# Kernel tuning notes

Hardware: AMD Instinct MI355X
Metric: run time of the kernel (lower is better)

The kernel has to match this reference:

```python
import jax, jax.numpy as jnp
import numpy as np

N_USERS = 100000
N_ITEMS = 50000
N = N_USERS + N_ITEMS
D = 64
N_LAYERS = 3
E = 3000000


def setup_inputs() -> dict:
    key = jax.random.key(0)
    k1, k2, k3, k4, k5 = jax.random.split(key, 5)
    rows = jax.random.randint(k1, (E,), 0, N, dtype=jnp.int32)
    cols = jax.random.randint(k2, (E,), 0, N, dtype=jnp.int32)
    vals = jax.random.uniform(k3, (E,), dtype=jnp.float32)
    user_emb = jax.random.normal(k4, (N_USERS, D), dtype=jnp.float32) * 0.1
    item_emb = jax.random.normal(k5, (N_ITEMS, D), dtype=jnp.float32) * 0.1
    return {"rows": rows, "cols": cols, "vals": vals,
            "user_emb": user_emb, "item_emb": item_emb}


def _spmm(rows, cols, vals, x):
    # sparse (COO) @ dense: out[r] += vals[e] * x[cols[e]]
    msgs = vals[:, None] * x[cols]  # [E, D]
    return jax.ops.segment_sum(msgs, rows, num_segments=N)


def reference(rows, cols, vals, user_emb, item_emb):
    all_emb = jnp.concatenate([user_emb, item_emb], axis=0)  # [N, D]
    acc = all_emb  # running sum over layer outputs (incl. layer 0)
    for _ in range(N_LAYERS):
        all_emb = _spmm(rows, cols, vals, all_emb)
        acc = acc + all_emb
    light_out = acc / (N_LAYERS + 1)  # mean over stacked layer embeddings
    users_final = light_out[:N_USERS]
    items_final = light_out[N_USERS:]
    return users_final, items_final
```

## Files before the change

### kernel.cpp

```cpp
#include <hip/hip_runtime.h>
#include <hip/hip_fp16.h>

#define N_USERS 100000
#define N_ITEMS 50000
#define N_TOT   150000
#define DIM     64
#define E_EDGES 3000000
#define NP1     (N_TOT + 1)
#define NB1     586
#define EPB     4096
#define SEDGE_MAX 4100000

__device__ __forceinline__ __half2 h2_from_int(int x) {
    union { int i; __half2 h; } u; u.i = x; return u.h;
}
__device__ __forceinline__ int int_from_h2(__half2 h) {
    union { int i; __half2 h; } u; u.h = h; return u.i;
}


__global__ void init_kernel(const float* __restrict__ user_emb,
                            const float* __restrict__ item_emb,
                            __half2* __restrict__ b0) {
    int i = blockIdx.x * blockDim.x + threadIdx.x;
    const int total4 = N_TOT * DIM / 4;
    if (i < total4) {
        int base = i * 4;
        float4 v = (base < N_USERS * DIM)
                     ? reinterpret_cast<const float4*>(user_emb)[i]
                     : reinterpret_cast<const float4*>(item_emb)[(base - N_USERS * DIM) >> 2];
        b0[i * 2]     = __floats2half2_rn(v.x, v.y);
        b0[i * 2 + 1] = __floats2half2_rn(v.z, v.w);
    }
}

__global__ void zero_int_kernel(int* __restrict__ p, int n) {
    int i = blockIdx.x * blockDim.x + threadIdx.x;
    if (i < n) p[i] = 0;
}


__global__ __launch_bounds__(256) void hist1_kernel(const int* __restrict__ rows,
                                                    int* __restrict__ hist1) {
    __shared__ int h[NB1];
    for (int b = threadIdx.x; b < NB1; b += 256) h[b] = 0;
    __syncthreads();
    int e0 = blockIdx.x * EPB;
    int cnt = min(EPB, E_EDGES - e0);
    for (int i = threadIdx.x; i < cnt; i += 256)
        atomicAdd(&h[rows[e0 + i] >> 8], 1);
    __syncthreads();
    for (int b = threadIdx.x; b < NB1; b += 256)
        if (h[b]) atomicAdd(&hist1[b], h[b]);
}

__global__ __launch_bounds__(256) void scan586_kernel(const int* __restrict__ src,
                                                      int* __restrict__ dst) {
    __shared__ int psum[256];
    int t = threadIdx.x;
    int i0 = t * 3;
    int s0 = (i0     < NB1) ? src[i0]     : 0;
    int s1 = (i0 + 1 < NB1) ? src[i0 + 1] : 0;
    int s2 = (i0 + 2 < NB1) ? src[i0 + 2] : 0;
    int tsum = s0 + s1 + s2;
    psum[t] = tsum;
    __syncthreads();
    for (int off = 1; off < 256; off <<= 1) {
        int x = (t >= off) ? psum[t - off] : 0;
        __syncthreads();
        psum[t] += x;
        __syncthreads();
    }
    int excl = psum[t] - tsum;
    if (i0     < NB1) dst[i0]     = excl;
    if (i0 + 1 < NB1) dst[i0 + 1] = excl + s0;
    if (i0 + 2 < NB1) dst[i0 + 2] = excl + s0 + s1;
    if (t == 255) dst[NB1] = psum[255];
}

__global__ __launch_bounds__(256) void bin_kernel(const int* __restrict__ rows,
                                                  const int* __restrict__ cols,
                                                  const float* __restrict__ vals,
                                                  const int* __restrict__ bstart,
                                                  int* __restrict__ fill1,
                                                  int2* __restrict__ tmp) {
    __shared__ int sw0[EPB];
    __shared__ int sw1[EPB];
    __shared__ unsigned short sbkt[EPB];
    __shared__ int hist[NB1];
    __shared__ int sstart[NB1];
    __shared__ int gbase[NB1];
    __shared__ int cursor[NB1];
    __shared__ int psum[256];

    int e0 = blockIdx.x * EPB;
    int cnt = min(EPB, E_EDGES - e0);

    for (int b = threadIdx.x; b < NB1; b += 256) hist[b] = 0;
    __syncthreads();

    int r[16], c[16]; float v[16];
#pragma unroll
    for (int k = 0; k < 16; ++k) {
        int i = threadIdx.x + k * 256;
        r[k] = -1;
        if (i < cnt) {
            int e = e0 + i;
            r[k] = rows[e];
            c[k] = cols[e];
            v[k] = vals[e];
            atomicAdd(&hist[r[k] >> 8], 1);
        }
    }
    __syncthreads();

    int t = threadIdx.x;
    int i0 = t * 3;
    int s0 = (i0     < NB1) ? hist[i0]     : 0;
    int s1 = (i0 + 1 < NB1) ? hist[i0 + 1] : 0;
    int s2 = (i0 + 2 < NB1) ? hist[i0 + 2] : 0;
    int tsum = s0 + s1 + s2;
    psum[t] = tsum;
    __syncthreads();
    for (int off = 1; off < 256; off <<= 1) {
        int x = (t >= off) ? psum[t - off] : 0;
        __syncthreads();
        psum[t] += x;
        __syncthreads();
    }
    int excl = psum[t] - tsum;
    if (i0     < NB1) sstart[i0]     = excl;
    if (i0 + 1 < NB1) sstart[i0 + 1] = excl + s0;
    if (i0 + 2 < NB1) sstart[i0 + 2] = excl + s0 + s1;
    __syncthreads();

    for (int b = threadIdx.x; b < NB1; b += 256) {
        int h = hist[b];
        gbase[b] = (h > 0) ? (bstart[b] + atomicAdd(&fill1[b], h)) : 0;
        cursor[b] = sstart[b];
    }
    __syncthreads();

#pragma unroll
    for (int k = 0; k < 16; ++k) {
        if (r[k] >= 0) {
            int b = r[k] >> 8;
            int p = atomicAdd(&cursor[b], 1);
            sw0[p] = ((r[k] & 0xFF) << 24) | c[k];
            sw1[p] = int_from_h2(__floats2half2_rn(v[k], v[k]));
            sbkt[p] = (unsigned short)b;
        }
    }
    __syncthreads();

    for (int i = threadIdx.x; i < cnt; i += 256) {
        int b = sbkt[i];
        int dest = gbase[b] + (i - sstart[b]);
        tmp[dest] = make_int2(sw0[i], sw1[i]);
    }
}

__global__ __launch_bounds__(256) void bukhist_kernel(const int2* __restrict__ tmp,
                                                      const int* __restrict__ bstart,
                                                      int* __restrict__ rowdeg,
                                                      int* __restrict__ bktpad) {
    int b = blockIdx.x;
    int beg = bstart[b], end = bstart[b + 1];
    __shared__ int hist[256];
    __shared__ int sp[256];
    int t = threadIdx.x;
    hist[t] = 0;
    __syncthreads();
    for (int i = beg + t; i < end; i += 256)
        atomicAdd(&hist[((unsigned)tmp[i].x) >> 24], 1);
    __syncthreads();
    int d = hist[t];
    int r = b * 256 + t;
    if (r < N_TOT) rowdeg[r] = d;
    sp[t] = (d + 7) & ~7;
    __syncthreads();
    for (int off = 128; off > 0; off >>= 1) {
        if (t < off) sp[t] += sp[t + off];
        __syncthreads();
    }
    if (t == 0) bktpad[b] = sp[0];
}

__global__ __launch_bounds__(256) void rowptr_kernel(const int* __restrict__ rowdeg,
                                                     const int* __restrict__ pbstart,
                                                     int* __restrict__ row_ptr,
                                                     int2* __restrict__ sedge) {
    int b = blockIdx.x, t = threadIdx.x;
    int r = b * 256 + t;
    int d = (r < N_TOT) ? rowdeg[r] : 0;
    int pd = (d + 7) & ~7;
    __shared__ int scn[256];
    scn[t] = pd;
    __syncthreads();
    for (int off = 1; off < 256; off <<= 1) {
        int x = (t >= off) ? scn[t - off] : 0;
        __syncthreads();
        scn[t] += x;
        __syncthreads();
    }
    int excl = scn[t] - pd;
    int rp = pbstart[b] + excl;
    if (r <= N_TOT) row_ptr[r] = rp;
    if (r < N_TOT) {
        int2* spad = sedge + rp + d;
        for (int i = d; i < pd; ++i) *spad++ = make_int2(0, 0);
    }
}

__global__ __launch_bounds__(256) void sort_kernel(const int2* __restrict__ tmp,
                                                   const int* __restrict__ bstart,
                                                   const int* __restrict__ row_ptr,
                                                   int2* __restrict__ sedge) {
    int b = blockIdx.x;
    int beg = bstart[b], end = bstart[b + 1];
    __shared__ int cursor[256];
    int t = threadIdx.x;
    int r = b * 256 + t;
    cursor[t] = (r < N_TOT) ? row_ptr[r] : 0;
    __syncthreads();
    for (int i = beg + t; i < end; i += 256) {
        int2 rec = tmp[i];
        int lr = ((unsigned)rec.x) >> 24;
        int p = atomicAdd(&cursor[lr], 1);
        sedge[p] = make_int2(rec.x & 0xFFFFFF, rec.y);
    }
}


__global__ __launch_bounds__(256) void spmm2_kernel(const int* __restrict__ row_ptr,
                                                    const int2* __restrict__ sedge,
                                                    const __half2* __restrict__ src,
                                                    __half2* __restrict__ dst,
                                                    const __half2* __restrict__ c0,
                                                    const __half2* __restrict__ c1,
                                                    float* __restrict__ acc,
                                                    int last) {
    int wid2 = (blockIdx.x * blockDim.x + threadIdx.x) >> 6;
    int lane = threadIdx.x & 63;
    int sub = lane & 31;
    int row = wid2 * 2 + (lane >> 5);
    if (row >= N_TOT) return;
    int beg = row_ptr[row];
    int ng  = (row_ptr[row + 1] - beg) >> 3;
    const int4* ep = reinterpret_cast<const int4*>(sedge + beg);
    float s0 = 0.0f, s1 = 0.0f;
    const __half2 z2 = __floats2half2_rn(0.0f, 0.0f);
    for (int g = 0; g < ng; ++g) {
        int4 e0 = ep[0]; int4 e1 = ep[1]; int4 e2 = ep[2]; int4 e3 = ep[3];
        ep += 4;
        __half2 a0 = z2, a1 = z2;
        a0 = __hfma2(h2_from_int(e0.y), src[(unsigned)e0.x * 32u + sub], a0);
        a1 = __hfma2(h2_from_int(e0.w), src[(unsigned)e0.z * 32u + sub], a1);
        a0 = __hfma2(h2_from_int(e1.y), src[(unsigned)e1.x * 32u + sub], a0);
        a1 = __hfma2(h2_from_int(e1.w), src[(unsigned)e1.z * 32u + sub], a1);
        a0 = __hfma2(h2_from_int(e2.y), src[(unsigned)e2.x * 32u + sub], a0);
        a1 = __hfma2(h2_from_int(e2.w), src[(unsigned)e2.z * 32u + sub], a1);
        a0 = __hfma2(h2_from_int(e3.y), src[(unsigned)e3.x * 32u + sub], a0);
        a1 = __hfma2(h2_from_int(e3.w), src[(unsigned)e3.z * 32u + sub], a1);
        float2 fa = __half22float2(__hadd2(a0, a1));
        s0 += fa.x; s1 += fa.y;
    }
    unsigned o = (unsigned)row * 32u + sub;
    if (last) {
        float2 f0 = __half22float2(c0[o]);
        float2 f1 = __half22float2(c1[o]);
        float2 f2 = __half22float2(src[o]);
        float2 rr;
        rr.x = (f0.x + f1.x + f2.x + s0) * 0.25f;
        rr.y = (f0.y + f1.y + f2.y + s1) * 0.25f;
        reinterpret_cast<float2*>(acc)[o] = rr;
    } else {
        dst[o] = __floats2half2_rn(s0, s1);
    }
}


__global__ void initf_kernel(const float* __restrict__ user_emb,
                             const float* __restrict__ item_emb,
                             float* __restrict__ cur,
                             float* __restrict__ acc) {
    int i = blockIdx.x * blockDim.x + threadIdx.x;
    const int total = N_TOT * DIM;
    if (i < total) {
        float v = (i < N_USERS * DIM) ? user_emb[i] : item_emb[i - N_USERS * DIM];
        cur[i] = v;
        acc[i] = v;
    }
}

__global__ void zero_f_kernel(float* __restrict__ p, int n) {
    int i = blockIdx.x * blockDim.x + threadIdx.x;
    if (i < n) p[i] = 0.0f;
}

__global__ void spmm_atomic_kernel(const int* __restrict__ rows, const int* __restrict__ cols,
                                   const float* __restrict__ vals,
                                   const float* __restrict__ cur, float* __restrict__ next) {
    int tid = blockIdx.x * blockDim.x + threadIdx.x;
    int e = tid >> 4;
    int q = (tid & 15) << 2;
    if (e < E_EDGES) {
        int r = rows[e];
        int c = cols[e];
        float v = vals[e];
        const float4 x = *reinterpret_cast<const float4*>(cur + (size_t)c * DIM + q);
        float* dstp = next + (size_t)r * DIM + q;
        atomicAdd(dstp + 0, v * x.x);
        atomicAdd(dstp + 1, v * x.y);
        atomicAdd(dstp + 2, v * x.z);
        atomicAdd(dstp + 3, v * x.w);
    }
}

__global__ void accum_kernel(float* __restrict__ acc, const float* __restrict__ next, int n) {
    int i = blockIdx.x * blockDim.x + threadIdx.x;
    if (i < n) acc[i] += next[i];
}

__global__ void scale_kernel(float* __restrict__ acc, int n) {
    int i = blockIdx.x * blockDim.x + threadIdx.x;
    if (i < n) acc[i] *= 0.25f;
}


extern "C" void kernel_launch(void* const* d_in, const int* in_sizes, int n_in,
                              void* d_out, int out_size, void* d_ws, size_t ws_size,
                              hipStream_t stream) {
    const int*   rows     = (const int*)d_in[0];
    const int*   cols     = (const int*)d_in[1];
    const float* vals     = (const float*)d_in[2];
    const float* user_emb = (const float*)d_in[3];
    const float* item_emb = (const float*)d_in[4];
    float* acc = (float*)d_out;

    const int total  = N_TOT * DIM;
    const int total2 = total / 2;
    const int tb = 256;

    __half2* b0 = (__half2*)d_ws;
    __half2* b1 = b0 + (size_t)total2;
    __half2* b2 = b1 + (size_t)total2;
    int2* tmp   = (int2*)d_ws;
    int2* sedge = (int2*)(b2 + (size_t)total2);
    int* row_ptr = (int*)(sedge + (size_t)SEDGE_MAX);
    int* rowdeg  = row_ptr + NP1;
    int* hist1   = rowdeg + N_TOT;
    int* fill1   = hist1 + NB1;
    int* bktpad  = fill1 + NB1;
    int* bstart  = bktpad + NB1;
    int* pbstart = bstart + NB1 + 1;
    size_t need = (size_t)((char*)(pbstart + NB1 + 1) - (char*)d_ws);

    const int grid_bin = (E_EDGES + EPB - 1) / EPB;

    if (ws_size >= need) {
        zero_int_kernel<<<(2 * NB1 + tb - 1) / tb, tb, 0, stream>>>(hist1, 2 * NB1);
        hist1_kernel<<<grid_bin, tb, 0, stream>>>(rows, hist1);
        scan586_kernel<<<1, tb, 0, stream>>>(hist1, bstart);
        bin_kernel<<<grid_bin, tb, 0, stream>>>(rows, cols, vals, bstart, fill1, tmp);
        bukhist_kernel<<<NB1, tb, 0, stream>>>(tmp, bstart, rowdeg, bktpad);
        scan586_kernel<<<1, tb, 0, stream>>>(bktpad, pbstart);
        rowptr_kernel<<<NB1, tb, 0, stream>>>(rowdeg, pbstart, row_ptr, sedge);
        sort_kernel<<<NB1, tb, 0, stream>>>(tmp, bstart, row_ptr, sedge);

        dim3 blkInit((total / 4 + tb - 1) / tb);
        init_kernel<<<blkInit, tb, 0, stream>>>(user_emb, item_emb, b0);

        const int waves = N_TOT / 2;
        dim3 blkRows((waves * 64 + tb - 1) / tb);
        spmm2_kernel<<<blkRows, tb, 0, stream>>>(row_ptr, sedge, b0, b1, b0, b0, acc, 0);
        spmm2_kernel<<<blkRows, tb, 0, stream>>>(row_ptr, sedge, b1, b2, b0, b0, acc, 0);
        spmm2_kernel<<<blkRows, tb, 0, stream>>>(row_ptr, sedge, b2, b2, b0, b1, acc, 1);
    } else {
        float* fcur = (float*)d_ws;
        float* fnxt = fcur + (size_t)total;
        dim3 blkTotal((total + tb - 1) / tb);
        initf_kernel<<<blkTotal, tb, 0, stream>>>(user_emb, item_emb, fcur, acc);
        const long long spmm_threads = (long long)E_EDGES * 16;
        dim3 blkSpmm((unsigned)((spmm_threads + tb - 1) / tb));
        for (int layer = 0; layer < 3; ++layer) {
            zero_f_kernel<<<blkTotal, tb, 0, stream>>>(fnxt, total);
            spmm_atomic_kernel<<<blkSpmm, tb, 0, stream>>>(rows, cols, vals, fcur, fnxt);
            accum_kernel<<<blkTotal, tb, 0, stream>>>(acc, fnxt, total);
            float* t = fcur; fcur = fnxt; fnxt = t;
        }
        scale_kernel<<<blkTotal, tb, 0, stream>>>(acc, total);
    }
}
```

Baseline: 299.4 us.

## Split sorted edges into column and half-value arrays, fuse rowptr with sort

Sorted edge storage changes from interleaved int2 (column plus duplicated half2 value) to separate int column and __half value arrays, cutting per-edge bytes from 8 to 6. The rowptr and sort kernels are merged into one kernel, dropping a launch and a re-read of row_ptr. The SpMM inner loop now handles two 8-edge groups per iteration with all 16 gathers issued before the FMAs, to expose more memory parallelism. The cost is extra value unpacking via low/high half broadcasts and higher register pressure.

```diff
diff --git a/kernel.cpp b/kernel.cpp
--- a/kernel.cpp
+++ b/kernel.cpp
@@ -10,13 +10,6 @@
 #define NB1     586
 #define EPB     4096
 #define SEDGE_MAX 4100000
-
-__device__ __forceinline__ __half2 h2_from_int(int x) {
-    union { int i; __half2 h; } u; u.i = x; return u.h;
-}
-__device__ __forceinline__ int int_from_h2(__half2 h) {
-    union { int i; __half2 h; } u; u.h = h; return u.i;
-}
 
 
 __global__ void init_kernel(const float* __restrict__ user_emb,
@@ -147,7 +140,7 @@
             int b = r[k] >> 8;
             int p = atomicAdd(&cursor[b], 1);
             sw0[p] = ((r[k] & 0xFF) << 24) | c[k];
-            sw1[p] = int_from_h2(__floats2half2_rn(v[k], v[k]));
+            sw1[p] = __float_as_int(v[k]);
             sbkt[p] = (unsigned short)b;
         }
     }
@@ -186,15 +179,19 @@
     if (t == 0) bktpad[b] = sp[0];
 }
 
-__global__ __launch_bounds__(256) void rowptr_kernel(const int* __restrict__ rowdeg,
-                                                     const int* __restrict__ pbstart,
-                                                     int* __restrict__ row_ptr,
-                                                     int2* __restrict__ sedge) {
+__global__ __launch_bounds__(256) void fsort_kernel(const int* __restrict__ rowdeg,
+                                                    const int* __restrict__ pbstart,
+                                                    const int* __restrict__ bstart,
+                                                    const int2* __restrict__ tmp,
+                                                    int* __restrict__ row_ptr,
+                                                    int* __restrict__ scol,
+                                                    __half* __restrict__ sval) {
     int b = blockIdx.x, t = threadIdx.x;
     int r = b * 256 + t;
     int d = (r < N_TOT) ? rowdeg[r] : 0;
     int pd = (d + 7) & ~7;
     __shared__ int scn[256];
+    __shared__ int cursor[256];
     scn[t] = pd;
     __syncthreads();
     for (int off = 1; off < 256; off <<= 1) {
@@ -206,34 +203,28 @@
     int excl = scn[t] - pd;
     int rp = pbstart[b] + excl;
     if (r <= N_TOT) row_ptr[r] = rp;
+    cursor[t] = rp;
     if (r < N_TOT) {
-        int2* spad = sedge + rp + d;
-        for (int i = d; i < pd; ++i) *spad++ = make_int2(0, 0);
-    }
-}
-
-__global__ __launch_bounds__(256) void sort_kernel(const int2* __restrict__ tmp,
-                                                   const int* __restrict__ bstart,
-                                                   const int* __restrict__ row_ptr,
-                                                   int2* __restrict__ sedge) {
-    int b = blockIdx.x;
+        for (int i = d; i < pd; ++i) {
+            scol[rp + i] = 0;
+            sval[rp + i] = __float2half_rn(0.0f);
+        }
+    }
+    __syncthreads();
     int beg = bstart[b], end = bstart[b + 1];
-    __shared__ int cursor[256];
-    int t = threadIdx.x;
-    int r = b * 256 + t;
-    cursor[t] = (r < N_TOT) ? row_ptr[r] : 0;
-    __syncthreads();
     for (int i = beg + t; i < end; i += 256) {
         int2 rec = tmp[i];
         int lr = ((unsigned)rec.x) >> 24;
         int p = atomicAdd(&cursor[lr], 1);
-        sedge[p] = make_int2(rec.x & 0xFFFFFF, rec.y);
+        scol[p] = rec.x & 0xFFFFFF;
+        sval[p] = __float2half_rn(__int_as_float(rec.y));
     }
 }
 
 
 __global__ __launch_bounds__(256) void spmm2_kernel(const int* __restrict__ row_ptr,
-                                                    const int2* __restrict__ sedge,
+                                                    const int* __restrict__ scol,
+                                                    const __half* __restrict__ sval,
                                                     const __half2* __restrict__ src,
                                                     __half2* __restrict__ dst,
                                                     const __half2* __restrict__ c0,
@@ -247,23 +238,80 @@
     if (row >= N_TOT) return;
     int beg = row_ptr[row];
     int ng  = (row_ptr[row + 1] - beg) >> 3;
-    const int4* ep = reinterpret_cast<const int4*>(sedge + beg);
+    const int4* cp = reinterpret_cast<const int4*>(scol + beg);
+    const int4* vp = reinterpret_cast<const int4*>(sval + beg);
     float s0 = 0.0f, s1 = 0.0f;
     const __half2 z2 = __floats2half2_rn(0.0f, 0.0f);
-    for (int g = 0; g < ng; ++g) {
-        int4 e0 = ep[0]; int4 e1 = ep[1]; int4 e2 = ep[2]; int4 e3 = ep[3];
-        ep += 4;
+
+    if (ng & 1) {
+        int4 ci0 = cp[0], ci1 = cp[1];
+        int4 vi  = vp[0];
+        cp += 2; vp += 1;
+        __half2 x0 = src[(unsigned)ci0.x * 32u + sub];
+        __half2 x1 = src[(unsigned)ci0.y * 32u + sub];
+        __half2 x2 = src[(unsigned)ci0.z * 32u + sub];
+        __half2 x3 = src[(unsigned)ci0.w * 32u + sub];
+        __half2 x4 = src[(unsigned)ci1.x * 32u + sub];
+        __half2 x5 = src[(unsigned)ci1.y * 32u + sub];
+        __half2 x6 = src[(unsigned)ci1.z * 32u + sub];
+        __half2 x7 = src[(unsigned)ci1.w * 32u + sub];
+        const __half2* hv = reinterpret_cast<const __half2*>(&vi);
         __half2 a0 = z2, a1 = z2;
-        a0 = __hfma2(h2_from_int(e0.y), src[(unsigned)e0.x * 32u + sub], a0);
-        a1 = __hfma2(h2_from_int(e0.w), src[(unsigned)e0.z * 32u + sub], a1);
-        a0 = __hfma2(h2_from_int(e1.y), src[(unsigned)e1.x * 32u + sub], a0);
-        a1 = __hfma2(h2_from_int(e1.w), src[(unsigned)e1.z * 32u + sub], a1);
-        a0 = __hfma2(h2_from_int(e2.y), src[(unsigned)e2.x * 32u + sub], a0);
-        a1 = __hfma2(h2_from_int(e2.w), src[(unsigned)e2.z * 32u + sub], a1);
-        a0 = __hfma2(h2_from_int(e3.y), src[(unsigned)e3.x * 32u + sub], a0);
-        a1 = __hfma2(h2_from_int(e3.w), src[(unsigned)e3.z * 32u + sub], a1);
+        a0 = __hfma2(__low2half2(hv[0]),  x0, a0);
+        a1 = __hfma2(__high2half2(hv[0]), x1, a1);
+        a0 = __hfma2(__low2half2(hv[1]),  x2, a0);
+        a1 = __hfma2(__high2half2(hv[1]), x3, a1);
+        a0 = __hfma2(__low2half2(hv[2]),  x4, a0);
+        a1 = __hfma2(__high2half2(hv[2]), x5, a1);
+        a0 = __hfma2(__low2half2(hv[3]),  x6, a0);
+        a1 = __hfma2(__high2half2(hv[3]), x7, a1);
         float2 fa = __half22float2(__hadd2(a0, a1));
         s0 += fa.x; s1 += fa.y;
+    }
+    int npair = ng >> 1;
+    for (int it = 0; it < npair; ++it) {
+        int4 ca = cp[0], cb = cp[1], cc = cp[2], cd = cp[3];
+        int4 va = vp[0], vb = vp[1];
+        cp += 4; vp += 2;
+        __half2 x0  = src[(unsigned)ca.x * 32u + sub];
+        __half2 x1  = src[(unsigned)ca.y * 32u + sub];
+        __half2 x2  = src[(unsigned)ca.z * 32u + sub];
+        __half2 x3  = src[(unsigned)ca.w * 32u + sub];
+        __half2 x4  = src[(unsigned)cb.x * 32u + sub];
+        __half2 x5  = src[(unsigned)cb.y * 32u + sub];
+        __half2 x6  = src[(unsigned)cb.z * 32u + sub];
+        __half2 x7  = src[(unsigned)cb.w * 32u + sub];
+        __half2 x8  = src[(unsigned)cc.x * 32u + sub];
+        __half2 x9  = src[(unsigned)cc.y * 32u + sub];
+        __half2 x10 = src[(unsigned)cc.z * 32u + sub];
+        __half2 x11 = src[(unsigned)cc.w * 32u + sub];
+        __half2 x12 = src[(unsigned)cd.x * 32u + sub];
+        __half2 x13 = src[(unsigned)cd.y * 32u + sub];
+        __half2 x14 = src[(unsigned)cd.z * 32u + sub];
+        __half2 x15 = src[(unsigned)cd.w * 32u + sub];
+        const __half2* hva = reinterpret_cast<const __half2*>(&va);
+        const __half2* hvb = reinterpret_cast<const __half2*>(&vb);
+        __half2 a0 = z2, a1 = z2, a2 = z2, a3 = z2;
+        a0 = __hfma2(__low2half2(hva[0]),  x0,  a0);
+        a1 = __hfma2(__high2half2(hva[0]), x1,  a1);
+        a0 = __hfma2(__low2half2(hva[1]),  x2,  a0);
+        a1 = __hfma2(__high2half2(hva[1]), x3,  a1);
+        a0 = __hfma2(__low2half2(hva[2]),  x4,  a0);
+        a1 = __hfma2(__high2half2(hva[2]), x5,  a1);
+        a0 = __hfma2(__low2half2(hva[3]),  x6,  a0);
+        a1 = __hfma2(__high2half2(hva[3]), x7,  a1);
+        a2 = __hfma2(__low2half2(hvb[0]),  x8,  a2);
+        a3 = __hfma2(__high2half2(hvb[0]), x9,  a3);
+        a2 = __hfma2(__low2half2(hvb[1]),  x10, a2);
+        a3 = __hfma2(__high2half2(hvb[1]), x11, a3);
+        a2 = __hfma2(__low2half2(hvb[2]),  x12, a2);
+        a3 = __hfma2(__high2half2(hvb[2]), x13, a3);
+        a2 = __hfma2(__low2half2(hvb[3]),  x14, a2);
+        a3 = __hfma2(__high2half2(hvb[3]), x15, a3);
+        float2 f01 = __half22float2(__hadd2(a0, a1));
+        float2 f23 = __half22float2(__hadd2(a2, a3));
+        s0 += f01.x + f23.x;
+        s1 += f01.y + f23.y;
     }
     unsigned o = (unsigned)row * 32u + sub;
     if (last) {
@@ -346,8 +394,9 @@
     __half2* b1 = b0 + (size_t)total2;
     __half2* b2 = b1 + (size_t)total2;
     int2* tmp   = (int2*)d_ws;
-    int2* sedge = (int2*)(b2 + (size_t)total2);
-    int* row_ptr = (int*)(sedge + (size_t)SEDGE_MAX);
+    int*    scol = (int*)(b2 + (size_t)total2);
+    __half* sval = (__half*)(scol + (size_t)SEDGE_MAX);
+    int* row_ptr = (int*)(sval + (size_t)SEDGE_MAX);
     int* rowdeg  = row_ptr + NP1;
     int* hist1   = rowdeg + N_TOT;
     int* fill1   = hist1 + NB1;
@@ -365,17 +414,17 @@
         bin_kernel<<<grid_bin, tb, 0, stream>>>(rows, cols, vals, bstart, fill1, tmp);
         bukhist_kernel<<<NB1, tb, 0, stream>>>(tmp, bstart, rowdeg, bktpad);
         scan586_kernel<<<1, tb, 0, stream>>>(bktpad, pbstart);
-        rowptr_kernel<<<NB1, tb, 0, stream>>>(rowdeg, pbstart, row_ptr, sedge);
-        sort_kernel<<<NB1, tb, 0, stream>>>(tmp, bstart, row_ptr, sedge);
+        fsort_kernel<<<NB1, tb, 0, stream>>>(rowdeg, pbstart, bstart, tmp,
+                                             row_ptr, scol, sval);
 
         dim3 blkInit((total / 4 + tb - 1) / tb);
         init_kernel<<<blkInit, tb, 0, stream>>>(user_emb, item_emb, b0);
 
         const int waves = N_TOT / 2;
         dim3 blkRows((waves * 64 + tb - 1) / tb);
-        spmm2_kernel<<<blkRows, tb, 0, stream>>>(row_ptr, sedge, b0, b1, b0, b0, acc, 0);
-        spmm2_kernel<<<blkRows, tb, 0, stream>>>(row_ptr, sedge, b1, b2, b0, b0, acc, 0);
-        spmm2_kernel<<<blkRows, tb, 0, stream>>>(row_ptr, sedge, b2, b2, b0, b1, acc, 1);
+        spmm2_kernel<<<blkRows, tb, 0, stream>>>(row_ptr, scol, sval, b0, b1, b0, b0, acc, 0);
+        spmm2_kernel<<<blkRows, tb, 0, stream>>>(row_ptr, scol, sval, b1, b2, b0, b0, acc, 0);
+        spmm2_kernel<<<blkRows, tb, 0, stream>>>(row_ptr, scol, sval, b2, b2, b0, b1, acc, 1);
     } else {
         float* fcur = (float*)d_ws;
         float* fnxt = fcur + (size_t)total;
```

Result: slower. 309.1 us (+3.2%).
